# Kernel tuning notes

Hardware: AMD Instinct MI355X
Metric: run time of the kernel (lower is better)

## Reference

```python
import jax, jax.numpy as jnp
import numpy as np

B, N, D, H, HD, T, E = 8, 8192, 1536, 4, 256, 50, 64
LN_EPS = 1e-5


def setup_inputs() -> dict:
    key = jax.random.key(0)
    ks = jax.random.split(key, 24)
    w = lambda k, shape, sc=0.02: (jax.random.normal(k, shape, jnp.float32) * sc)
    return {
        'features': jax.random.normal(ks[0], (B, N, D), jnp.float32),
        'attn_mask': jnp.ones((B, N), dtype=bool),
        'tissue_id': jax.random.randint(ks[1], (B,), 0, T),
        # ABMIL params (heads stacked on leading axis)
        'attW': w(ks[2], (H, D, HD)), 'attb': jnp.zeros((H, HD), jnp.float32),
        'gateW': w(ks[3], (H, D, HD)), 'gateb': jnp.zeros((H, HD), jnp.float32),
        'brW': w(ks[4], (H, HD)), 'brb': jnp.zeros((H,), jnp.float32),
        'condW': w(ks[5], (H * D, D)), 'condb': jnp.zeros((D,), jnp.float32),
        # shared feature extractor: Linear(D,256) + LayerNorm(256)
        'sfW': w(ks[6], (D, 256)), 'sfb': jnp.zeros((256,), jnp.float32),
        'sfg': jnp.ones((256,), jnp.float32), 'sfbeta': jnp.zeros((256,), jnp.float32),
        # hypernetwork: Embedding(T,E) -> Linear(E,64) -> GELU -> Linear(64,257)
        'temb': w(ks[7], (T, E), 1.0),
        'h1W': w(ks[8], (E, 64)), 'h1b': jnp.zeros((64,), jnp.float32),
        'h2W': w(ks[9], (64, 257), 0.001), 'h2b': jnp.zeros((257,), jnp.float32),
    }


def _layernorm(x, g, b):
    mu = jnp.mean(x, axis=-1, keepdims=True)
    var = jnp.mean((x - mu) ** 2, axis=-1, keepdims=True)
    return (x - mu) * jax.lax.rsqrt(var + LN_EPS) * g + b


def reference(features, attn_mask, tissue_id, attW, attb, gateW, gateb,
              brW, brb, condW, condb, sfW, sfb, sfg, sfbeta,
              temb, h1W, h1b, h2W, h2b):
    # --- ABMIL gated multi-head tanh-attention pooling (dropout is eval/no-op) ---
    a = jnp.tanh(jnp.einsum('bnd,hdk->bhnk', features, attW) + attb[:, None, :])      # [B,H,N,HD]
    g = jax.nn.sigmoid(jnp.einsum('bnd,hdk->bhnk', features, gateW) + gateb[:, None, :])
    scores = jnp.einsum('bhnk,hk->bhn', a * g, brW) + brb[None, :, None]               # [B,H,N]
    scores = jnp.where(attn_mask[:, None, :], scores, jnp.float32(-1e9))
    attn = jax.nn.softmax(scores, axis=-1)                                             # over instances
    pooled = jnp.einsum('bhn,bnd->bhd', attn, features).reshape(B, H * D)              # concat heads
    M = pooled @ condW + condb                                                          # [B,D]

    # --- shared feature extractor ---
    sh = jax.nn.gelu(_layernorm(M @ sfW + sfb, sfg, sfbeta), approximate=False)         # [B,256]

    # --- tissue hypernetwork: per-sample dynamic linear head ---
    te = temb[tissue_id]                                                                # [B,E]
    hp = jax.nn.gelu(te @ h1W + h1b, approximate=False) @ h2W + h2b                     # [B,257]
    y_pred = jnp.sum(sh * hp[:, :256], axis=-1) + hp[:, 256]                            # [B]

    head_attentions = scores[:, None, :, :]                                             # [B,1,H,N] (b r h n)
    return y_pred, head_attentions
```

## Files before the change

### kernel.cpp

```cpp
#include <hip/hip_runtime.h>


typedef unsigned short u16;
typedef unsigned int u32;
typedef __attribute__((ext_vector_type(8))) short bf16x8;
typedef __attribute__((ext_vector_type(4))) float f32x4;
typedef __attribute__((ext_vector_type(4))) float float4v;
typedef __attribute__((ext_vector_type(4))) u16 u16x4;

__device__ __forceinline__ u16 f2bf(float x) {
  u32 u = __float_as_uint(x);
  u32 r = (u + 0x7fffu + ((u >> 16) & 1u)) >> 16;
  return (u16)r;
}
__device__ __forceinline__ float bf2f(u16 v) { return __uint_as_float(((u32)v) << 16); }

__device__ __forceinline__ void async_copy16(void* lds, const void* g) {
  __builtin_amdgcn_global_load_lds((const __attribute__((address_space(1))) u32*)g,
                                   (__attribute__((address_space(3))) u32*)lds, 16, 0, 0);
}
__device__ __forceinline__ float fsigm(float x) { return 1.f / (1.f + __expf(-x)); }
__device__ __forceinline__ float ftanh(float x) {
  x = fminf(fmaxf(x, -15.f), 15.f);
  float e = __expf(2.f * x);
  return (e - 1.f) / (e + 1.f);
}
__device__ __forceinline__ float gelu_exact(float x) {
  return 0.5f * x * (1.f + erff(x * 0.70710678118654752f));
}


__global__ void zero_kernel(float* __restrict__ p, int n) {
  int i = blockIdx.x * 256 + threadIdx.x;
  if (i < n) p[i] = 0.f;
}

__global__ void convert_kernel(const float* __restrict__ f, u16* __restrict__ o, long n4) {
  long stride = (long)gridDim.x * blockDim.x;
  for (long i = blockIdx.x * (long)blockDim.x + threadIdx.x; i < n4; i += stride) {
    float4v v = ((const float4v*)f)[i];
    u16x4 r;
    r[0] = f2bf(v[0]); r[1] = f2bf(v[1]); r[2] = f2bf(v[2]); r[3] = f2bf(v[3]);
    ((u16x4*)o)[i] = r;
  }
}

__global__ void pack_kernel(const float* __restrict__ attW, const float* __restrict__ gateW,
                            u16* __restrict__ Bp) {
  int idx = blockIdx.x * 256 + threadIdx.x;
  int c = idx / 393216;
  int r = idx - c * 393216;
  int col = r / 1536;
  int d = r - col * 1536;
  int h = c >> 1;
  int k = ((c & 1) << 7) + (col >> 1);
  const float* W = (col & 1) ? gateW : attW;
  Bp[idx] = f2bf(W[(h * 1536 + d) * 256 + k]);
}

#define SYNCV(n) asm volatile("s_waitcnt vmcnt(" #n ")\n\ts_barrier" ::: "memory")

__global__ __launch_bounds__(512, 2)
void gemm_scores_kernel(const u16* __restrict__ A, const u16* __restrict__ Bp,
                        const float* __restrict__ attb, const float* __restrict__ gateb,
                        const float* __restrict__ brW, float* __restrict__ scores)
{
  __shared__ u16 lds[4][2][8192];

  const int tid = threadIdx.x;
  const int lane = tid & 63;
  const int wid = tid >> 6;
  const int wm = wid >> 2;
  const int wn = wid & 3;
  const int tileM = blockIdx.x >> 3;
  const int chunk = blockIdx.x & 7;
  const int tid8 = tid * 8;

  const int srow = tid >> 2;
  const int sk8 = (tid & 3) ^ ((srow >> 1) & 3);
  const u16* aS0 = A + ((long)(tileM * 256 + srow)) * 1536 + sk8 * 8;
  const u16* aS1 = aS0 + 128L * 1536;
  const u16* bS0 = Bp + (long)chunk * 393216 + (long)srow * 1536 + sk8 * 8;
  const u16* bS1 = bS0 + 128L * 1536;

  int aOff[8], bOff[4];
#pragma unroll
  for (int m = 0; m < 8; ++m) {
    int r = wm * 128 + m * 16 + (lane & 15);
    aOff[m] = r * 32 + (((lane >> 4) ^ ((r >> 1) & 3)) << 3);
  }
#pragma unroll
  for (int n = 0; n < 4; ++n) {
    int c = wn * 64 + n * 16 + (lane & 15);
    bOff[n] = c * 32 + (((lane >> 4) ^ ((c >> 1) & 3)) << 3);
  }

  f32x4 acc[8][4] = {};

#define STAGE(SUB, P0, P1, P2, P3, OFF)                  \
  do {                                                   \
    async_copy16(&lds[SUB][0][tid8], (P0) + (OFF));      \
    async_copy16(&lds[SUB][0][4096 + tid8], (P1) + (OFF)); \
    async_copy16(&lds[SUB][1][tid8], (P2) + (OFF));      \
    async_copy16(&lds[SUB][1][4096 + tid8], (P3) + (OFF)); \
  } while (0)

#define PHASE_BODY(SUB, DO_STAGE, SSUB, SOFF, SYNC)                              \
  do {                                                                           \
    SYNC;                                                                        \
    bf16x8 bfr[4], af[8];                                                        \
    _Pragma("unroll")                                                            \
    for (int n = 0; n < 4; ++n) bfr[n] = *(const bf16x8*)&lds[SUB][1][bOff[n]];  \
    _Pragma("unroll")                                                            \
    for (int m = 0; m < 8; ++m) af[m] = *(const bf16x8*)&lds[SUB][0][aOff[m]];   \
    if (DO_STAGE) STAGE(SSUB, sa0, sa1, sb0, sb1, SOFF);                         \
    __builtin_amdgcn_s_setprio(1);                                               \
    _Pragma("unroll")                                                            \
    for (int m = 0; m < 8; ++m)                                                  \
      _Pragma("unroll")                                                          \
      for (int n = 0; n < 4; ++n)                                                \
        acc[m][n] = __builtin_amdgcn_mfma_f32_16x16x32_bf16(af[m], bfr[n], acc[m][n], 0, 0, 0); \
    __builtin_amdgcn_s_setprio(0);                                               \
  } while (0)

  STAGE(0, aS0, aS1, bS0, bS1, 0);
  STAGE(1, aS0, aS1, bS0, bS1, 32);
  STAGE(2, aS0, aS1, bS0, bS1, 64);

  const u16 *sa0 = aS0 + 96, *sa1 = aS1 + 96, *sb0 = bS0 + 96, *sb1 = bS1 + 96;

  for (int it = 0; it < 11; ++it) {
    PHASE_BODY(0, true, 3, 0, SYNCV(8));
    PHASE_BODY(1, true, 0, 32, SYNCV(8));
    PHASE_BODY(2, true, 1, 64, SYNCV(8));
    PHASE_BODY(3, true, 2, 96, SYNCV(8));
    sa0 += 128; sa1 += 128; sb0 += 128; sb1 += 128;
  }
  PHASE_BODY(0, true, 3, 0, SYNCV(8));
  PHASE_BODY(1, false, 0, 0, SYNCV(8));
  PHASE_BODY(2, false, 0, 0, SYNCV(4));
  PHASE_BODY(3, false, 0, 0, SYNCV(0));

  const int h = chunk >> 1;
  const int k0 = (chunk & 1) << 7;
  float brw[4], bia[4];
  int par[4];
#pragma unroll
  for (int n = 0; n < 4; ++n) {
    int c = wn * 64 + n * 16 + (lane & 15);
    int k = k0 + (c >> 1);
    par[n] = c & 1;
    brw[n] = brW[h * 256 + k];
    bia[n] = par[n] ? gateb[h * 256 + k] : attb[h * 256 + k];
  }
#pragma unroll
  for (int m = 0; m < 8; ++m) {
#pragma unroll
    for (int i = 0; i < 4; ++i) {
      float s = 0.f;
#pragma unroll
      for (int n = 0; n < 4; ++n) {
        float v = acc[m][n][i] + bia[n];
        float t = par[n] ? fsigm(v) : ftanh(v);
        float tp = __shfl_xor(t, 1);
        s += par[n] ? 0.f : t * tp * brw[n];
      }
      s += __shfl_xor(s, 1);
      s += __shfl_xor(s, 2);
      s += __shfl_xor(s, 4);
      s += __shfl_xor(s, 8);
      if ((lane & 15) == 0) {
        int row = tileM * 256 + wm * 128 + m * 16 + ((lane >> 4) << 2) + i;
        int b = row >> 13;
        int n_ = row & 8191;
        atomicAdd(&scores[((b << 2) + h) * 8192 + n_], s);
      }
    }
  }
#undef STAGE
#undef PHASE_BODY
}

__global__ __launch_bounds__(512)
void softmax_kernel(const float* __restrict__ scores, const float* __restrict__ brb,
                    float* __restrict__ attn, float* __restrict__ ha)
{
  const int bh = blockIdx.x;
  const float bb = brb[bh & 3];
  const long base = (long)bh * 8192;
  const int t = threadIdx.x;
  const int lane = t & 63, wid = t >> 6;
  __shared__ float red[8];
  float v[16];
  float mx = -1e30f;
#pragma unroll
  for (int i = 0; i < 16; ++i) {
    v[i] = scores[base + t + i * 512] + bb;
    mx = fmaxf(mx, v[i]);
  }
#pragma unroll
  for (int o = 1; o < 64; o <<= 1) mx = fmaxf(mx, __shfl_xor(mx, o));
  if (lane == 0) red[wid] = mx;
  __syncthreads();
#pragma unroll
  for (int w = 0; w < 8; ++w) mx = fmaxf(mx, red[w]);
  __syncthreads();
  float sum = 0.f;
#pragma unroll
  for (int i = 0; i < 16; ++i) {
    float sc = v[i];
    ha[base + t + i * 512] = sc;
    float e = __expf(sc - mx);
    v[i] = e;
    sum += e;
  }
#pragma unroll
  for (int o = 1; o < 64; o <<= 1) sum += __shfl_xor(sum, o);
  if (lane == 0) red[wid] = sum;
  __syncthreads();
  sum = 0.f;
#pragma unroll
  for (int w = 0; w < 8; ++w) sum += red[w];
  float inv = 1.f / sum;
#pragma unroll
  for (int i = 0; i < 16; ++i) attn[base + t + i * 512] = v[i] * inv;
}

__global__ __launch_bounds__(256)
void pooled_kernel(const u16* __restrict__ fbf, const float* __restrict__ attn,
                   float* __restrict__ pooled)
{
  __shared__ float aw[4][256];
  const int t = threadIdx.x;
  const int b = blockIdx.x >> 5;
  const int nc = blockIdx.x & 31;
#pragma unroll
  for (int h = 0; h < 4; ++h) aw[h][t] = attn[((b << 2) + h) * 8192 + nc * 256 + t];
  __syncthreads();
  float acc[6][4] = {};
  const u16* basep = fbf + ((long)(b * 8192 + nc * 256)) * 1536;
  for (int n = 0; n < 256; ++n) {
    const u16* fr = basep + (long)n * 1536;
    float a0 = aw[0][n], a1 = aw[1][n], a2 = aw[2][n], a3 = aw[3][n];
#pragma unroll
    for (int j = 0; j < 6; ++j) {
      float f = bf2f(fr[t + j * 256]);
      acc[j][0] += a0 * f;
      acc[j][1] += a1 * f;
      acc[j][2] += a2 * f;
      acc[j][3] += a3 * f;
    }
  }
#pragma unroll
  for (int j = 0; j < 6; ++j)
#pragma unroll
    for (int h = 0; h < 4; ++h)
      atomicAdd(&pooled[((b << 2) + h) * 1536 + j * 256 + t], acc[j][h]);
}

__global__ __launch_bounds__(256)
void cond_kernel(const float* __restrict__ pooled, const float* __restrict__ condW,
                 const float* __restrict__ condb, float* __restrict__ M)
{
  __shared__ float pl[8 * 192];
  const int t = threadIdx.x;
  const int dc = blockIdx.x % 6;
  const int ks = blockIdx.x / 6;
  const int k0 = ks * 192;
  for (int i = t; i < 8 * 192; i += 256) {
    int b = i / 192, kk = i - b * 192;
    pl[i] = pooled[b * 6144 + k0 + kk];
  }
  __syncthreads();
  const int d = dc * 256 + t;
  float acc[8] = {};
  for (int kk = 0; kk < 192; ++kk) {
    float w = condW[(long)(k0 + kk) * 1536 + d];
#pragma unroll
    for (int b = 0; b < 8; ++b) acc[b] += pl[b * 192 + kk] * w;
  }
  if (ks == 0) {
    float cb = condb[d];
#pragma unroll
    for (int b = 0; b < 8; ++b) acc[b] += cb;
  }
#pragma unroll
  for (int b = 0; b < 8; ++b) atomicAdd(&M[b * 1536 + d], acc[b]);
}

__global__ __launch_bounds__(256)
void sf_kernel(const float* __restrict__ M, const float* __restrict__ sfW,
               const float* __restrict__ sfb, const float* __restrict__ sfg,
               const float* __restrict__ sfbeta, float* __restrict__ sh)
{
  __shared__ float mr[1536];
  __shared__ float red[4];
  const int b = blockIdx.x;
  const int c = threadIdx.x;
  const int lane = c & 63, wid = c >> 6;
  for (int i = c; i < 1536; i += 256) mr[i] = M[b * 1536 + i];
  __syncthreads();
  float acc = sfb[c];
  for (int k = 0; k < 1536; ++k) acc += mr[k] * sfW[k * 256 + c];
  float s = acc;
#pragma unroll
  for (int o = 1; o < 64; o <<= 1) s += __shfl_xor(s, o);
  if (lane == 0) red[wid] = s;
  __syncthreads();
  float mu = (red[0] + red[1] + red[2] + red[3]) * (1.f / 256.f);
  __syncthreads();
  float dv = (acc - mu) * (acc - mu);
#pragma unroll
  for (int o = 1; o < 64; o <<= 1) dv += __shfl_xor(dv, o);
  if (lane == 0) red[wid] = dv;
  __syncthreads();
  float var = (red[0] + red[1] + red[2] + red[3]) * (1.f / 256.f);
  float xn = (acc - mu) * rsqrtf(var + 1e-5f) * sfg[c] + sfbeta[c];
  sh[b * 256 + c] = gelu_exact(xn);
}

__global__ __launch_bounds__(320)
void head_kernel(const float* __restrict__ sh, const int* __restrict__ tissue,
                 const float* __restrict__ temb, const float* __restrict__ h1W,
                 const float* __restrict__ h1b, const float* __restrict__ h2W,
                 const float* __restrict__ h2b, float* __restrict__ y)
{
  __shared__ float hid[64];
  __shared__ float hp[257];
  __shared__ float red[5];
  const int t = threadIdx.x;
  const int lane = t & 63, wid = t >> 6;
  for (int b = 0; b < 8; ++b) {
    const int tix = tissue[b];
    if (t < 64) {
      float s = h1b[t];
      for (int e = 0; e < 64; ++e) s += temb[tix * 64 + e] * h1W[e * 64 + t];
      hid[t] = gelu_exact(s);
    }
    __syncthreads();
    if (t < 257) {
      float s = h2b[t];
      for (int j = 0; j < 64; ++j) s += hid[j] * h2W[j * 257 + t];
      hp[t] = s;
    }
    __syncthreads();
    float p = (t < 256) ? sh[b * 256 + t] * hp[t] : 0.f;
#pragma unroll
    for (int o = 1; o < 64; o <<= 1) p += __shfl_xor(p, o);
    if (lane == 0) red[wid] = p;
    __syncthreads();
    if (t == 0) y[b] = red[0] + red[1] + red[2] + red[3] + red[4] + hp[256];
    __syncthreads();
  }
}


extern "C" void kernel_launch(void* const* d_in, const int* in_sizes, int n_in,
                              void* d_out, int out_size, void* d_ws, size_t ws_size,
                              hipStream_t stream) {
  const float* features = (const float*)d_in[0];
  const int* tissue     = (const int*)d_in[2];
  const float* attW     = (const float*)d_in[3];
  const float* attb     = (const float*)d_in[4];
  const float* gateW    = (const float*)d_in[5];
  const float* gateb    = (const float*)d_in[6];
  const float* brW      = (const float*)d_in[7];
  const float* brb      = (const float*)d_in[8];
  const float* condW    = (const float*)d_in[9];
  const float* condb    = (const float*)d_in[10];
  const float* sfW      = (const float*)d_in[11];
  const float* sfb      = (const float*)d_in[12];
  const float* sfg      = (const float*)d_in[13];
  const float* sfbeta   = (const float*)d_in[14];
  const float* temb     = (const float*)d_in[15];
  const float* h1W      = (const float*)d_in[16];
  const float* h1b      = (const float*)d_in[17];
  const float* h2W      = (const float*)d_in[18];
  const float* h2b      = (const float*)d_in[19];

  char* ws = (char*)d_ws;
  u16* fbf      = (u16*)ws;
  u16* Bp       = (u16*)(ws + 201326592);
  float* scores = (float*)(ws + 207618048);
  float* pooled = (float*)(ws + 208666624);
  float* Mbuf   = (float*)(ws + 208863232);
  float* attn   = (float*)(ws + 208912384);
  float* shb    = (float*)(ws + 209960960);

  float* yout = (float*)d_out;
  float* haout = (float*)d_out + 8;

  zero_kernel<<<1264, 256, 0, stream>>>(scores, 323584);
  convert_kernel<<<2048, 256, 0, stream>>>(features, fbf, 25165824L);
  pack_kernel<<<12288, 256, 0, stream>>>(attW, gateW, Bp);
  gemm_scores_kernel<<<2048, 512, 0, stream>>>(fbf, Bp, attb, gateb, brW, scores);
  softmax_kernel<<<32, 512, 0, stream>>>(scores, brb, attn, haout);
  pooled_kernel<<<256, 256, 0, stream>>>(fbf, attn, pooled);
  cond_kernel<<<192, 256, 0, stream>>>(pooled, condW, condb, Mbuf);
  sf_kernel<<<8, 256, 0, stream>>>(Mbuf, sfW, sfb, sfg, sfbeta, shb);
  head_kernel<<<1, 320, 0, stream>>>(shb, tissue, temb, h1W, h1b, h2W, h2b, yout);
}
```

Measured before the change: 817.1 us.

## Restructure scores GEMM into double-buffered half-tile pipeline and vectorize pooled loads

The scores GEMM K-loop moves from a 4-stage single-sub-tile ring to a 2-buffer scheme. Each buffer holds two K-slices, and each slice's MFMA work is split into two halves. The loads for the next buffer are interleaved between explicit barriers, lgkmcnt waits and sched_barriers. The aim is to overlap global-to-LDS copies with MFMA issue at finer granularity, at the cost of twice as many barriers and less prefetch depth. The pooled kernel now uses 384 threads, each loading 4 contiguous bf16 values with one vector load instead of 6 strided scalar loads.

```diff
diff --git a/kernel.cpp b/kernel.cpp
--- a/kernel.cpp
+++ b/kernel.cpp
@@ -58,14 +58,18 @@
   Bp[idx] = f2bf(W[(h * 1536 + d) * 256 + k]);
 }
 
-#define SYNCV(n) asm volatile("s_waitcnt vmcnt(" #n ")\n\ts_barrier" ::: "memory")
+
+#define BARR __builtin_amdgcn_s_barrier()
+#define LGKM0 do { asm volatile("s_waitcnt lgkmcnt(0)" ::: "memory"); \
+                   __builtin_amdgcn_sched_barrier(0); } while (0)
+#define VMC(n) asm volatile("s_waitcnt vmcnt(" #n ")" ::: "memory")
 
 __global__ __launch_bounds__(512, 2)
 void gemm_scores_kernel(const u16* __restrict__ A, const u16* __restrict__ Bp,
                         const float* __restrict__ attb, const float* __restrict__ gateb,
                         const float* __restrict__ brW, float* __restrict__ scores)
 {
-  __shared__ u16 lds[4][2][8192];
+  __shared__ u16 lds[2][4][8192];
 
   const int tid = threadIdx.x;
   const int lane = tid & 63;
@@ -97,49 +101,68 @@
 
   f32x4 acc[8][4] = {};
 
-#define STAGE(SUB, P0, P1, P2, P3, OFF)                  \
-  do {                                                   \
-    async_copy16(&lds[SUB][0][tid8], (P0) + (OFF));      \
-    async_copy16(&lds[SUB][0][4096 + tid8], (P1) + (OFF)); \
-    async_copy16(&lds[SUB][1][tid8], (P2) + (OFF));      \
-    async_copy16(&lds[SUB][1][4096 + tid8], (P3) + (OFF)); \
+#define STG(NB, HALF, P0_, P1_, OFF)                                 \
+  do {                                                               \
+    async_copy16(&lds[NB][HALF][tid8], (P0_) + (OFF));               \
+    async_copy16(&lds[NB][HALF][4096 + tid8], (P1_) + (OFF));        \
   } while (0)
 
-#define PHASE_BODY(SUB, DO_STAGE, SSUB, SOFF, SYNC)                              \
-  do {                                                                           \
-    SYNC;                                                                        \
-    bf16x8 bfr[4], af[8];                                                        \
-    _Pragma("unroll")                                                            \
-    for (int n = 0; n < 4; ++n) bfr[n] = *(const bf16x8*)&lds[SUB][1][bOff[n]];  \
-    _Pragma("unroll")                                                            \
-    for (int m = 0; m < 8; ++m) af[m] = *(const bf16x8*)&lds[SUB][0][aOff[m]];   \
-    if (DO_STAGE) STAGE(SSUB, sa0, sa1, sb0, sb1, SOFF);                         \
-    __builtin_amdgcn_s_setprio(1);                                               \
-    _Pragma("unroll")                                                            \
-    for (int m = 0; m < 8; ++m)                                                  \
-      _Pragma("unroll")                                                          \
-      for (int n = 0; n < 4; ++n)                                                \
-        acc[m][n] = __builtin_amdgcn_mfma_f32_16x16x32_bf16(af[m], bfr[n], acc[m][n], 0, 0, 0); \
-    __builtin_amdgcn_s_setprio(0);                                               \
+#define MFMA16(MB)                                                                         \
+  do {                                                                                     \
+    __builtin_amdgcn_s_setprio(1);                                                         \
+    _Pragma("unroll")                                                                      \
+    for (int m = 0; m < 4; ++m)                                                            \
+      _Pragma("unroll")                                                                    \
+      for (int n = 0; n < 4; ++n)                                                          \
+        acc[(MB) + m][n] =                                                                 \
+            __builtin_amdgcn_mfma_f32_16x16x32_bf16(af[m], bfr[n], acc[(MB) + m][n], 0, 0, 0); \
+    __builtin_amdgcn_s_setprio(0);                                                         \
+    __builtin_amdgcn_sched_barrier(0);                                                     \
   } while (0)
 
-  STAGE(0, aS0, aS1, bS0, bS1, 0);
-  STAGE(1, aS0, aS1, bS0, bS1, 32);
-  STAGE(2, aS0, aS1, bS0, bS1, 64);
-
-  const u16 *sa0 = aS0 + 96, *sa1 = aS1 + 96, *sb0 = bS0 + 96, *sb1 = bS1 + 96;
-
-  for (int it = 0; it < 11; ++it) {
-    PHASE_BODY(0, true, 3, 0, SYNCV(8));
-    PHASE_BODY(1, true, 0, 32, SYNCV(8));
-    PHASE_BODY(2, true, 1, 64, SYNCV(8));
-    PHASE_BODY(3, true, 2, 96, SYNCV(8));
-    sa0 += 128; sa1 += 128; sb0 += 128; sb1 += 128;
-  }
-  PHASE_BODY(0, true, 3, 0, SYNCV(8));
-  PHASE_BODY(1, false, 0, 0, SYNCV(8));
-  PHASE_BODY(2, false, 0, 0, SYNCV(4));
-  PHASE_BODY(3, false, 0, 0, SYNCV(0));
+#define TILE(BUF, DOSTG, KO, VM1, VM3)                                              \
+  do {                                                                              \
+    bf16x8 bfr[4], af[4];                                                           \
+                                                                  \
+    _Pragma("unroll")                                                               \
+    for (int n = 0; n < 4; ++n) bfr[n] = *(const bf16x8*)&lds[BUF][1][bOff[n]];     \
+    _Pragma("unroll")                                                               \
+    for (int m = 0; m < 4; ++m) af[m] = *(const bf16x8*)&lds[BUF][0][aOff[m]];      \
+    if (DOSTG) STG((BUF) ^ 1, 0, aS0, aS1, KO);                                     \
+    BARR; LGKM0; MFMA16(0); BARR;                                                   \
+                                                 \
+    _Pragma("unroll")                                                               \
+    for (int m = 0; m < 4; ++m) af[m] = *(const bf16x8*)&lds[BUF][0][aOff[m + 4]];  \
+    if (DOSTG) STG((BUF) ^ 1, 1, bS0, bS1, KO);                                     \
+    BARR; LGKM0; MFMA16(4); VM1; BARR;                                              \
+                                                                  \
+    _Pragma("unroll")                                                               \
+    for (int n = 0; n < 4; ++n) bfr[n] = *(const bf16x8*)&lds[BUF][3][bOff[n]];     \
+    _Pragma("unroll")                                                               \
+    for (int m = 0; m < 4; ++m) af[m] = *(const bf16x8*)&lds[BUF][2][aOff[m]];      \
+    if (DOSTG) STG((BUF) ^ 1, 2, aS0, aS1, (KO) + 32);                              \
+    BARR; LGKM0; MFMA16(0); BARR;                                                   \
+                                                                  \
+    _Pragma("unroll")                                                               \
+    for (int m = 0; m < 4; ++m) af[m] = *(const bf16x8*)&lds[BUF][2][aOff[m + 4]];  \
+    if (DOSTG) STG((BUF) ^ 1, 3, bS0, bS1, (KO) + 32);                              \
+    BARR; LGKM0; MFMA16(4); VM3; BARR;                                              \
+  } while (0)
+
+  STG(0, 0, aS0, aS1, 0);
+  STG(0, 1, bS0, bS1, 0);
+  STG(0, 2, aS0, aS1, 32);
+  STG(0, 3, bS0, bS1, 32);
+  VMC(4);
+  BARR;
+
+  for (int t2 = 0; t2 < 11; ++t2) {
+    const int ko1 = (t2 * 2 + 1) * 64;
+    TILE(0, 1, ko1, VMC(4), VMC(4));
+    TILE(1, 1, ko1 + 64, VMC(4), VMC(4));
+  }
+  TILE(0, 1, 23 * 64, VMC(4), VMC(4));
+  TILE(1, 0, 0, VMC(0), (void)0);
 
   const int h = chunk >> 1;
   const int k0 = (chunk & 1) << 7;
@@ -177,8 +200,9 @@
       }
     }
   }
-#undef STAGE
-#undef PHASE_BODY
+#undef STG
+#undef MFMA16
+#undef TILE
 }
 
 __global__ __launch_bounds__(512)
@@ -226,7 +250,7 @@
   for (int i = 0; i < 16; ++i) attn[base + t + i * 512] = v[i] * inv;
 }
 
-__global__ __launch_bounds__(256)
+__global__ __launch_bounds__(384)
 void pooled_kernel(const u16* __restrict__ fbf, const float* __restrict__ attn,
                    float* __restrict__ pooled)
 {
@@ -234,17 +258,17 @@
   const int t = threadIdx.x;
   const int b = blockIdx.x >> 5;
   const int nc = blockIdx.x & 31;
-#pragma unroll
-  for (int h = 0; h < 4; ++h) aw[h][t] = attn[((b << 2) + h) * 8192 + nc * 256 + t];
-  __syncthreads();
-  float acc[6][4] = {};
-  const u16* basep = fbf + ((long)(b * 8192 + nc * 256)) * 1536;
+  for (int i = t; i < 1024; i += 384)
+    aw[i >> 8][i & 255] = attn[((b << 2) + (i >> 8)) * 8192 + nc * 256 + (i & 255)];
+  __syncthreads();
+  float acc[4][4] = {};
+  const u16* basep = fbf + ((long)(b * 8192 + nc * 256)) * 1536 + t * 4;
   for (int n = 0; n < 256; ++n) {
-    const u16* fr = basep + (long)n * 1536;
+    u16x4 v = *(const u16x4*)(basep + (long)n * 1536);
     float a0 = aw[0][n], a1 = aw[1][n], a2 = aw[2][n], a3 = aw[3][n];
 #pragma unroll
-    for (int j = 0; j < 6; ++j) {
-      float f = bf2f(fr[t + j * 256]);
+    for (int j = 0; j < 4; ++j) {
+      float f = bf2f(v[j]);
       acc[j][0] += a0 * f;
       acc[j][1] += a1 * f;
       acc[j][2] += a2 * f;
@@ -252,10 +276,10 @@
     }
   }
 #pragma unroll
-  for (int j = 0; j < 6; ++j)
+  for (int j = 0; j < 4; ++j)
 #pragma unroll
     for (int h = 0; h < 4; ++h)
-      atomicAdd(&pooled[((b << 2) + h) * 1536 + j * 256 + t], acc[j][h]);
+      atomicAdd(&pooled[((b << 2) + h) * 1536 + t * 4 + j], acc[j][h]);
 }
 
 __global__ __launch_bounds__(256)
@@ -395,7 +419,7 @@
   pack_kernel<<<12288, 256, 0, stream>>>(attW, gateW, Bp);
   gemm_scores_kernel<<<2048, 512, 0, stream>>>(fbf, Bp, attb, gateb, brW, scores);
   softmax_kernel<<<32, 512, 0, stream>>>(scores, brb, attn, haout);
-  pooled_kernel<<<256, 256, 0, stream>>>(fbf, attn, pooled);
+  pooled_kernel<<<256, 384, 0, stream>>>(fbf, attn, pooled);
   cond_kernel<<<192, 256, 0, stream>>>(pooled, condW, condb, Mbuf);
   sf_kernel<<<8, 256, 0, stream>>>(Mbuf, sfW, sfb, sfg, sfbeta, shb);
   head_kernel<<<1, 320, 0, stream>>>(shb, tissue, temb, h1W, h1b, h2W, h2b, yout);
```

New measurement: 797.6 us. 1.02x faster.
